# Kernel optimization log

Hardware: AMD Instinct MI355X
Metric: run time of the kernel (lower is better)

Reference implementation:

```python
import jax, jax.numpy as jnp
import numpy as np
from jax import lax

B, S, T = 32, 400, 100
V, OOV = 32000, 100
E, U, AU, GP, ENC = 512, 256, 256, 256, 512


def setup_inputs() -> dict:
    key = jax.random.key(0)
    ks = jax.random.split(key, 24)
    r = lambda k, shp: 0.02 * jax.random.normal(k, shp, dtype=jnp.float32)
    inp = {
        "gt_tokens": jax.random.randint(ks[0], (B, T), 0, V, dtype=jnp.int32),
        "extended_input_tokens": jax.random.randint(ks[1], (B, S), 0, V + OOV, dtype=jnp.int32),
        "enc_output": jax.random.normal(ks[2], (B, S, ENC), dtype=jnp.float32),
        "enc_attn": jax.random.normal(ks[3], (B, S, AU), dtype=jnp.float32),
        "h0": jnp.zeros((B, U), jnp.float32),
        "c0": jnp.zeros((B, U), jnp.float32),
        # learned parameters
        "emb": r(ks[4], (V, E)),
        "lstm_kernel": r(ks[5], (E, 4 * U)),
        "lstm_rec": r(ks[6], (U, 4 * U)),
        "lstm_bias": jnp.zeros((4 * U,), jnp.float32),
        "attn_Wd": r(ks[7], (2 * U, AU)),
        "attn_bd": jnp.zeros((AU,), jnp.float32),
        "attn_Wc": r(ks[8], (1, AU)),
        "attn_Wa": r(ks[9], (AU, 1)),
        "clf_W1": r(ks[10], (U, U)),
        "clf_b1": jnp.zeros((U,), jnp.float32),
        "clf_W2": r(ks[11], (U, V)),
        "clf_b2": jnp.zeros((V,), jnp.float32),
        "gp_Ws": r(ks[12], (2 * U, GP)),
        "gp_Wc": r(ks[13], (ENC, GP)),
        "gp_Wi": r(ks[14], (E, GP)),
        "gp_bi": jnp.zeros((GP,), jnp.float32),
        "gp_Wg": r(ks[15], (GP, 1)),
    }
    return inp


def _decode(gt_tokens, extended_input_tokens, enc_output, enc_attn, h0, c0,
            emb, lstm_kernel, lstm_rec, lstm_bias, attn_Wd, attn_bd, attn_Wc,
            attn_Wa, clf_W1, clf_b1, clf_W2, clf_b2, gp_Ws, gp_Wc, gp_Wi,
            gp_bi, gp_Wg):
    Bn, Sn = extended_input_tokens.shape
    gt_vec = emb[gt_tokens]                      # [B,T,E] teacher-forced inputs
    xs = jnp.swapaxes(gt_vec, 0, 1)              # [T,B,E]
    batch_idx = jnp.arange(Bn)[:, None]

    def step(carry, x):
        h, c, cov = carry                        # [B,U],[B,U],[B,S]
        # single-step LSTM (TF gate order i,f,g,o)
        z = x @ lstm_kernel + h @ lstm_rec + lstm_bias
        i_, f_, g_, o_ = jnp.split(z, 4, axis=-1)
        c = jax.nn.sigmoid(f_) * c + jax.nn.sigmoid(i_) * jnp.tanh(g_)
        h = jax.nn.sigmoid(o_) * jnp.tanh(c)
        dec_state = jnp.concatenate([h, c], axis=1)          # [B,2U]
        # Bahdanau attention with coverage
        dec_attn = dec_state @ attn_Wd + attn_bd             # [B,AU]
        cov_attn = cov[:, :, None] * attn_Wc[0]              # [B,S,AU]
        scores = jnp.tanh(enc_attn + cov_attn + dec_attn[:, None, :]) @ attn_Wa
        a = jax.nn.softmax(scores, axis=1)[:, :, 0]          # [B,S]
        c_vec = jnp.einsum('bse,bs->be', enc_output, a)      # [B,ENC]
        cov_loss = jnp.sum(jnp.minimum(cov, a), axis=1)      # [B]
        cov = cov + a
        # pg: faithful scalar quirk ([0,0,0] of broadcast sum in original)
        g = dec_state[0] @ gp_Ws + c_vec[0] @ gp_Wc + (x[0] @ gp_Wi + gp_bi)
        pg = jax.nn.sigmoid((g @ gp_Wg)[0])
        # vocab distribution, extended with OOV zeros
        vocab_p = jax.nn.softmax((h @ clf_W1 + clf_b1) @ clf_W2 + clf_b2, axis=-1)
        vocab_p = jnp.concatenate([vocab_p, jnp.zeros((Bn, OOV), vocab_p.dtype)], axis=1)
        # copy distribution via scatter-add of attention onto extended ids
        sent_p = jnp.zeros((Bn, V + OOV), a.dtype).at[batch_idx, extended_input_tokens].add(a)
        final = pg * vocab_p + (1.0 - pg) * sent_p           # [B,V+OOV]
        tok = jnp.argmax(final, axis=1).astype(jnp.int32)
        return (h, c, cov), (final, tok, cov_loss)

    cov0 = jnp.zeros((Bn, Sn), jnp.float32)
    _, (probs, seqs, cov_losses) = lax.scan(step, (h0, c0, cov0), xs)
    return (jnp.swapaxes(probs, 0, 1),       # [B,T,V+OOV]
            jnp.swapaxes(seqs, 0, 1),        # [B,T]
            jnp.swapaxes(cov_losses, 0, 1))  # [B,T]


def reference(gt_tokens, extended_input_tokens, enc_output, enc_attn, h0, c0,
              emb, lstm_kernel, lstm_rec, lstm_bias, attn_Wd, attn_bd,
              attn_Wc, attn_Wa, clf_W1, clf_b1, clf_W2, clf_b2, gp_Ws, gp_Wc,
              gp_Wi, gp_bi, gp_Wg):
    return _decode(gt_tokens, extended_input_tokens, enc_output, enc_attn, h0,
                   c0, emb, lstm_kernel, lstm_rec, lstm_bias, attn_Wd,
                   attn_bd, attn_Wc, attn_Wa, clf_W1, clf_b1, clf_W2, clf_b2,
                   gp_Ws, gp_Wc, gp_Wi, gp_bi, gp_Wg)
```

## Files before the change

### kernel.cpp

```cpp
#include <hip/hip_runtime.h>
#include <hip/hip_bf16.h>

#define Bn 32
#define Sn 400
#define Tn 100
#define Vn 32000
#define OOVn 100
#define VEn 32100
#define En 512
#define Un 256
#define AUn 256
#define GPn 256
#define ENCn 512
#define Z4n 1024
#define NPB 250

typedef __attribute__((ext_vector_type(8))) short bf16x8;
typedef __attribute__((ext_vector_type(4))) float f32x4;
typedef unsigned short ushort_t;
typedef unsigned long long u64;

__device__ __forceinline__ float rcp_f(float x){ return __builtin_amdgcn_rcpf(x); }
__device__ __forceinline__ float tanh_fast(float x){
  float e2 = __expf(2.f*x);
  return 1.f - 2.f*rcp_f(e2 + 1.f);
}
__device__ __forceinline__ float sigmoid_f(float x){ return 1.f/(1.f+__expf(-x)); }
__device__ __forceinline__ ushort_t f2bf(float f){
  unsigned u = __float_as_uint(f);
  unsigned r = (u + 0x7FFFu + ((u>>16)&1u)) >> 16;
  return (ushort_t)r;
}
__device__ __forceinline__ u64 shfl_xor_u64(u64 v, int m){
  unsigned lo = (unsigned)v, hi = (unsigned)(v>>32);
  lo = (unsigned)__shfl_xor((int)lo, m);
  hi = (unsigned)__shfl_xor((int)hi, m);
  return ((u64)hi<<32)|(u64)lo;
}

__device__ __forceinline__ void st_rlx(float* p, float v){
  __hip_atomic_store(p, v, __ATOMIC_RELAXED, __HIP_MEMORY_SCOPE_AGENT);
}
__device__ __forceinline__ float ld_rlx(const float* p){
  return __hip_atomic_load(p, __ATOMIC_RELAXED, __HIP_MEMORY_SCOPE_AGENT);
}
__device__ __forceinline__ void st_rlxu(unsigned* p, unsigned v){
  __hip_atomic_store(p, v, __ATOMIC_RELAXED, __HIP_MEMORY_SCOPE_AGENT);
}
__device__ __forceinline__ void st_rlx64(u64* p, u64 v){
  __hip_atomic_store(p, v, __ATOMIC_RELAXED, __HIP_MEMORY_SCOPE_AGENT);
}
__device__ __forceinline__ u64 ld_rlx64(const u64* p){
  return __hip_atomic_load(p, __ATOMIC_RELAXED, __HIP_MEMORY_SCOPE_AGENT);
}
__device__ __forceinline__ void st_flag(unsigned* p, unsigned v){
  __hip_atomic_store(p, v, __ATOMIC_RELAXED, __HIP_MEMORY_SCOPE_AGENT);
}
__device__ __forceinline__ unsigned ld_flag(const unsigned* p){
  return __hip_atomic_load(p, __ATOMIC_RELAXED, __HIP_MEMORY_SCOPE_AGENT);
}


__global__ __launch_bounds__(256) void k_zx(const int* __restrict__ gt,
    const float* __restrict__ emb, const float* __restrict__ Wk,
    const float* __restrict__ bias, float* __restrict__ Zx,
    const float* __restrict__ W2, ushort_t* __restrict__ W2T,
    unsigned* __restrict__ bars, unsigned* __restrict__ bars2,
    float* __restrict__ covloss){
  __shared__ __align__(16) char zbuf[16640];
  float (*As)[17] = (float(*)[17])zbuf;
  float (*Bs)[65] = (float(*)[65])(zbuf + 4352);
  int*   tok_lds  = (int*)(zbuf + 4352 + 4160);
  int r0 = blockIdx.x * 64;
  int c0 = blockIdx.y * 64;
  int tid = threadIdx.x;
  int ty = tid >> 4, tx16 = tid & 15;
  if (blockIdx.x == 0){
    int y = blockIdx.y;
    #pragma unroll
    for (int i = 0; i < 2; ++i){
      int idx = y*512 + i*256 + tid;
      bars[idx] = 0u;
      if (idx < NPB*32) bars2[idx] = 0u;
    }
    if (tid < 200) covloss[y*200 + tid] = 0.f;
  }
  if (tid < 64){
    int r = r0 + tid;
    tok_lds[tid] = gt[(r & 31)*Tn + (r >> 5)];
  }
  __syncthreads();
  float acc[4][4] = {};
  for (int k0 = 0; k0 < En; k0 += 16){
    #pragma unroll
    for (int p = 0; p < 4; ++p){
      int row = (tid>>4) + p*16, kk = tid & 15;
      As[row][kk] = emb[(size_t)tok_lds[row]*En + k0 + kk];
    }
    #pragma unroll
    for (int p = 0; p < 4; ++p){
      int kk = (tid>>6) + p*4, cc = tid & 63;
      Bs[kk][cc] = Wk[(size_t)(k0+kk)*Z4n + c0 + cc];
    }
    __syncthreads();
    #pragma unroll
    for (int kk = 0; kk < 16; ++kk){
      float av[4], bv[4];
      #pragma unroll
      for (int i=0;i<4;++i) av[i] = As[ty*4+i][kk];
      #pragma unroll
      for (int j=0;j<4;++j) bv[j] = Bs[kk][tx16*4+j];
      #pragma unroll
      for (int i=0;i<4;++i)
        #pragma unroll
        for (int j=0;j<4;++j) acc[i][j] += av[i]*bv[j];
    }
    __syncthreads();
  }
  #pragma unroll
  for (int i=0;i<4;++i){
    int row = r0 + ty*4 + i;
    #pragma unroll
    for (int j=0;j<4;++j){
      int col = c0 + tx16*4 + j;
      Zx[(size_t)row*Z4n + col] = acc[i][j] + bias[col];
    }
  }
  float (*tl)[65] = (float(*)[65])zbuf;
  int tx = tid & 63, ty4 = tid >> 6;
  int bid = blockIdx.x*16 + blockIdx.y;
  for (int rep = 0; rep < 3; ++rep){
    int tile = bid + rep*800;
    if (tile >= 2000) break;
    int n0 = (tile % 500) * 64, k0 = (tile / 500) * 64;
    __syncthreads();
    #pragma unroll
    for (int i = 0; i < 16; ++i){
      int kk = ty4 + i*4;
      tl[kk][tx] = W2[(size_t)(k0+kk)*Vn + n0 + tx];
    }
    __syncthreads();
    #pragma unroll
    for (int i = 0; i < 16; ++i){
      int n = ty4 + i*4;
      W2T[(size_t)(n0+n)*Un + k0 + tx] = f2bf(tl[tx][n]);
    }
  }
}


__global__ __launch_bounds__(1024, 1) void k_loop(
    const float* __restrict__ Zx, const float* __restrict__ Wr,
    const float* __restrict__ Wd, const float* __restrict__ bd,
    const float* __restrict__ Wc, const float* __restrict__ Wa,
    const float* __restrict__ enc_attn,
    const float* __restrict__ h0, const float* __restrict__ c0,
    float* __restrict__ h_all, float* __restrict__ decp,
    float* __restrict__ c0_all, float* __restrict__ a_all,
    float* __restrict__ covloss, float* __restrict__ spart,
    unsigned* __restrict__ bars){
  __shared__ float Wr_lds[256*128];
  __shared__ float hfull[Un];
  __shared__ float ppart[8][132];
  __shared__ float zx_lds[128];
  __shared__ float zfull[128];
  __shared__ float hnew[32], cown[32];
  __shared__ float dec_lds[AUn];
  __shared__ float cov_lds[50], sc_lds[50];
  __shared__ float wred[16];
  __shared__ float red8[8];

  const int b = blockIdx.x & 31, k = blockIdx.x >> 5;
  const int tid = threadIdx.x, lane = tid & 63, w = tid >> 6;
  unsigned* flags = bars + b*8*32;
  unsigned* myflag = flags + k*32;

  for (int idx = tid; idx < 256*128; idx += 1024){
    int u = idx >> 7, jl = idx & 127;
    int gcol = 32*k + (jl & 31) + 256*(jl >> 5);
    Wr_lds[idx] = Wr[(size_t)u*Z4n + gcol];
  }
  if (tid < 32) cown[tid] = c0[b*Un + 32*k + tid];
  if (tid < 50) cov_lds[tid] = 0.f;
  const float4 wc4 = *(const float4*)(Wc + lane*4);
  const float4 wa4 = *(const float4*)(Wa + lane*4);
  if (tid < 256) hfull[tid] = h0[b*Un + tid];
  if (tid >= 256 && tid < 384){
    int jl = tid - 256;
    int gcol = 32*k + (jl & 31) + 256*(jl >> 5);
    zx_lds[jl] = Zx[(size_t)(0*Bn + b)*Z4n + gcol];
  }
  __syncthreads();

  {
    int p = tid >> 7, jl = tid & 127;
    float acc = 0.f;
    const float* wr = Wr_lds + (p*32)*128 + jl;
    const float* hb = hfull + p*32;
    #pragma unroll 8
    for (int uu = 0; uu < 32; ++uu) acc += hb[uu]*wr[uu*128];
    ppart[p][jl] = acc;
  }
  __syncthreads();
  if (tid < 128){
    float s = zx_lds[tid];
    #pragma unroll
    for (int q = 0; q < 8; ++q) s += ppart[q][tid];
    zfull[tid] = s;
  }
  __syncthreads();
  if (tid < 32){
    float zi = zfull[tid], zf = zfull[32+tid], zg = zfull[64+tid], zo = zfull[96+tid];
    float cn = sigmoid_f(zf)*cown[tid] + sigmoid_f(zi)*tanhf(zg);
    float hn = sigmoid_f(zo)*tanhf(cn);
    cown[tid] = cn; hnew[tid] = hn;
    int col = 32*k + tid;
    st_rlx(h_all + (size_t)(0*Bn + b)*Un + col, hn);
    if (b == 0) c0_all[0*Un + col] = cn;
  }
  __syncthreads();
  if (tid < 256){
    int c = tid;
    float acc = 0.f;
    const float* wdh = Wd + (size_t)(32*k)*AUn + c;
    #pragma unroll 8
    for (int u = 0; u < 32; ++u) acc += hnew[u]*wdh[(size_t)u*AUn];
    const float* wdc = Wd + (size_t)(Un + 32*k)*AUn + c;
    #pragma unroll 8
    for (int u = 0; u < 32; ++u) acc += cown[u]*wdc[(size_t)u*AUn];
    st_rlx(decp + (size_t)(b*8 + k)*256 + c, acc);
  }
  __syncthreads();
  if (tid == 0) st_flag(myflag, 1u);

  for (int t = 0; t < Tn; ++t){
    const int cur = t & 1, oth = cur ^ 1;
    if (tid < 8){
      while (ld_flag(flags + tid*32) < (unsigned)(t+1))
        __builtin_amdgcn_s_sleep(1);
    }
    __syncthreads();
    if (tid < 256){
      hfull[tid] = ld_rlx(h_all + (size_t)(t*Bn + b)*Un + tid);
    } else if (tid < 512){
      int c = tid - 256;
      float s = bd[c];
      const float* dp = decp + (size_t)cur*(Bn*8*256) + (size_t)(b*8)*256 + c;
      #pragma unroll
      for (int q = 0; q < 8; ++q) s += ld_rlx(dp + q*256);
      dec_lds[c] = s;
    } else if (tid < 520){
      red8[tid-512] = (t > 0) ? ld_rlx(spart + oth*(Bn*8) + b*8 + (tid-512)) : 0.f;
    } else if (tid >= 576 && tid < 704 && t + 1 < Tn){
      int jl = tid - 576;
      int gcol = 32*k + (jl & 31) + 256*(jl >> 5);
      zx_lds[jl] = Zx[(size_t)((t+1)*Bn + b)*Z4n + gcol];
    }
    __syncthreads();
    if (t > 0 && w == 0){
      float pv = (lane < 8) ? red8[lane] : 0.f;
      pv += __shfl_xor(pv, 1); pv += __shfl_xor(pv, 2); pv += __shfl_xor(pv, 4);
      float inv = 1.f / __shfl(pv, 0);
      float clp = 0.f;
      if (lane < 50){
        float aa = sc_lds[lane] * inv;
        float co = cov_lds[lane];
        a_all[(size_t)((t-1)*Bn + b)*Sn + 50*k + lane] = aa;
        clp = fminf(co, aa);
        cov_lds[lane] = co + aa;
      }
      #pragma unroll
      for (int m = 1; m < 64; m <<= 1) clp += __shfl_xor(clp, m);
      if (lane == 0) atomicAdd(&covloss[b*Tn + (t-1)], clp);
    }
    {
      int p = tid >> 7, jl = tid & 127;
      float acc = 0.f;
      const float* wr = Wr_lds + (p*32)*128 + jl;
      const float* hb = hfull + p*32;
      #pragma unroll 8
      for (int uu = 0; uu < 32; ++uu) acc += hb[uu]*wr[uu*128];
      ppart[p][jl] = acc;
    }
    __syncthreads();
    if (tid < 128 && t + 1 < Tn){
      float s = zx_lds[tid];
      #pragma unroll
      for (int q = 0; q < 8; ++q) s += ppart[q][tid];
      zfull[tid] = s;
    }
    __syncthreads();
    if (tid < 32 && t + 1 < Tn){
      float zi = zfull[tid], zf = zfull[32+tid], zg = zfull[64+tid], zo = zfull[96+tid];
      float cn = sigmoid_f(zf)*cown[tid] + sigmoid_f(zi)*tanhf(zg);
      float hn = sigmoid_f(zo)*tanhf(cn);
      cown[tid] = cn; hnew[tid] = hn;
      int col = 32*k + tid;
      st_rlx(h_all + (size_t)((t+1)*Bn + b)*Un + col, hn);
      if (b == 0) c0_all[(t+1)*Un + col] = cn;
    }
    __syncthreads();
    if (w < 4){
      if (t + 1 < Tn){
        int c = tid;
        float acc = 0.f;
        const float* wdh = Wd + (size_t)(32*k)*AUn + c;
        #pragma unroll 8
        for (int u = 0; u < 32; ++u) acc += hnew[u]*wdh[(size_t)u*AUn];
        const float* wdc = Wd + (size_t)(Un + 32*k)*AUn + c;
        #pragma unroll 8
        for (int u = 0; u < 32; ++u) acc += cown[u]*wdc[(size_t)u*AUn];
        st_rlx(decp + (size_t)oth*(Bn*8*256) + (size_t)(b*8 + k)*256 + c, acc);
      }
    } else {
      const float4 da = *(const float4*)(dec_lds + lane*4);
      float wsum = 0.f;
      for (int sl = w - 4; sl < 50; sl += 12){
        float cvv = cov_lds[sl];
        const float4 e = *(const float4*)(enc_attn + ((size_t)(b*Sn + 50*k + sl))*AUn + lane*4);
        float psc = tanh_fast(e.x + cvv*wc4.x + da.x)*wa4.x
                  + tanh_fast(e.y + cvv*wc4.y + da.y)*wa4.y
                  + tanh_fast(e.z + cvv*wc4.z + da.z)*wa4.z
                  + tanh_fast(e.w + cvv*wc4.w + da.w)*wa4.w;
        #pragma unroll
        for (int m = 1; m < 64; m <<= 1) psc += __shfl_xor(psc, m);
        if (lane == 0){
          float ev = __expf(psc);
          sc_lds[sl] = ev;
          wsum += ev;
        }
      }
      if (lane == 0) wred[w] = wsum;
    }
    __syncthreads();
    if (tid == 0){
      float S = 0.f;
      #pragma unroll
      for (int q = 4; q < 16; ++q) S += wred[q];
      st_rlx(spart + cur*(Bn*8) + b*8 + k, S);
    }
    __syncthreads();
    if (tid == 0) st_flag(myflag, (unsigned)(t + 2));
  }

  if (tid < 8){
    while (ld_flag(flags + tid*32) < (unsigned)(Tn + 1))
      __builtin_amdgcn_s_sleep(1);
  }
  __syncthreads();
  if (tid < 8) red8[tid] = ld_rlx(spart + ((Tn-1)&1)*(Bn*8) + b*8 + tid);
  __syncthreads();
  if (w == 0){
    float pv = (lane < 8) ? red8[lane] : 0.f;
    pv += __shfl_xor(pv, 1); pv += __shfl_xor(pv, 2); pv += __shfl_xor(pv, 4);
    float inv = 1.f / __shfl(pv, 0);
    float clp = 0.f;
    if (lane < 50){
      float aa = sc_lds[lane] * inv;
      float co = cov_lds[lane];
      a_all[(size_t)((Tn-1)*Bn + b)*Sn + 50*k + lane] = aa;
      clp = fminf(co, aa);
    }
    #pragma unroll
    for (int m = 1; m < 64; m <<= 1) clp += __shfl_xor(clp, m);
    if (lane == 0) atomicAdd(&covloss[b*Tn + (Tn-1)], clp);
  }
}


__global__ __launch_bounds__(512, 1) void k_post(
    const float* __restrict__ h_all, const float* __restrict__ W1,
    const float* __restrict__ b1, ushort_t* __restrict__ hid,
    const int* __restrict__ gt, const float* __restrict__ emb,
    const float* __restrict__ gpWi, const float* __restrict__ gpbi,
    const float* __restrict__ a_all, const float* __restrict__ enc_out,
    const float* __restrict__ c0_all, const float* __restrict__ gpWs,
    const float* __restrict__ gpWc, const float* __restrict__ gpWg,
    float* __restrict__ pg, const ushort_t* __restrict__ W2T,
    const float* __restrict__ b2, float* __restrict__ Sp,
    float* __restrict__ Ssum, u64* __restrict__ Ap,
    float* __restrict__ probs, unsigned* __restrict__ bars2){
  __shared__ __align__(16) char sb[135168];
  __shared__ float red4[4];
  const int gid = blockIdx.x, tid = threadIdx.x;
  const int lane = tid & 63, w = tid >> 6;
  unsigned* myflag = bars2 + gid*32;

  if (gid < 100){
    int t = gid;
    float* hl = (float*)sb;
    for (int i = tid; i < Bn*Un; i += 512) hl[i] = h_all[(size_t)t*Bn*Un + i];
    __syncthreads();
    int j = tid & 255, p = tid >> 8;
    float bj = b1[j];
    float acc[16];
    #pragma unroll
    for (int i = 0; i < 16; ++i) acc[i] = bj;
    for (int u = 0; u < Un; ++u){
      float wv = W1[u*Un + j];
      const float* hp = hl + (p*16)*Un + u;
      #pragma unroll
      for (int i = 0; i < 16; ++i) acc[i] += hp[i*Un] * wv;
    }
    __syncthreads();
    ushort_t* hidL = (ushort_t*)sb;
    #pragma unroll
    for (int i = 0; i < 16; ++i) hidL[(p*16+i)*Un + j] = f2bf(acc[i]);
    __syncthreads();
    unsigned* hw = (unsigned*)hid + (size_t)t*4096;
    const unsigned* hs = (const unsigned*)hidL;
    for (int i = tid; i < 4096; i += 512) st_rlxu(hw + i, hs[i]);
  } else if (gid < 200){
    int t = gid - 100;
    float* al = (float*)sb;
    float* cv = al + 400;
    float* xl = cv + 512;
    for (int s = tid; s < Sn; s += 512) al[s] = a_all[(size_t)(t*Bn)*Sn + s];
    for (int i = tid; i < En; i += 512) xl[i] = emb[(size_t)gt[t]*En + i];
    __syncthreads();
    if (tid < ENCn){
      float acc = 0.f;
      for (int s = 0; s < Sn; ++s) acc += enc_out[(size_t)s*ENCn + tid]*al[s];
      cv[tid] = acc;
    }
    __syncthreads();
    if (tid < 256){
      int j = tid;
      float g = gpbi[j];
      for (int u = 0; u < En; ++u) g += xl[u]*gpWi[u*GPn + j];
      const float* h0r = h_all + (size_t)t*Bn*Un;
      const float* c0r = c0_all + t*Un;
      for (int u = 0; u < Un; ++u) g += h0r[u]*gpWs[u*GPn + j];
      for (int u = 0; u < Un; ++u) g += c0r[u]*gpWs[(Un+u)*GPn + j];
      for (int e = 0; e < ENCn; ++e) g += cv[e]*gpWc[e*GPn + j];
      float v = g * gpWg[j];
      #pragma unroll
      for (int m = 1; m < 64; m <<= 1) v += __shfl_xor(v, m);
      if (lane == 0) red4[w] = v;
    }
    __syncthreads();
    if (tid == 0)
      st_rlx(&pg[t], 1.f/(1.f+__expf(-(red4[0]+red4[1]+red4[2]+red4[3]))));
  }
  __syncthreads();
  if (tid == 0) st_flag(myflag, 1u);
  if (tid < NPB){ while (ld_flag(bars2 + tid*32) < 1u) __builtin_amdgcn_s_sleep(1); }
  __syncthreads();

  ushort_t* Bs = (ushort_t*)sb;
  const int slice = gid % 125, gx = gid / 125;
  const int n0 = slice * 256;
  {
    int rr = tid >> 1, half = (tid & 1) * 128;
    const ushort_t* gb = W2T + (size_t)(n0 + rr)*Un + half;
    ushort_t* lb = Bs + rr*264 + half;
    #pragma unroll
    for (int j2 = 0; j2 < 16; ++j2)
      *((uint4*)lb + j2) = *((const uint4*)gb + j2);
  }
  __syncthreads();
  const int cbase = gx ? 13 : 0;
  const int nch   = gx ? 12 : 13;

  for (int ci = 0; ci < nch; ++ci){
    int r0 = (cbase + ci) * 128;
    bf16x8 af[8];
    {
      const ushort_t* ar = hid + (size_t)(r0 + w*16 + (lane&15))*Un + (lane>>4)*8;
      #pragma unroll
      for (int kk = 0; kk < 8; ++kk) af[kk] = *(const bf16x8*)(ar + kk*32);
    }
    f32x4 acc[16];
    #pragma unroll
    for (int i = 0; i < 16; ++i) acc[i] = (f32x4){0.f,0.f,0.f,0.f};
    #pragma unroll
    for (int kk = 0; kk < 8; ++kk){
      #pragma unroll
      for (int nt = 0; nt < 16; ++nt){
        bf16x8 bf = *(const bf16x8*)(Bs + (nt*16 + (lane&15))*264 + kk*32 + (lane>>4)*8);
        acc[nt] = __builtin_amdgcn_mfma_f32_16x16x32_bf16(af[kk], bf, acc[nt], 0, 0, 0);
      }
    }
    float rs[4] = {0.f,0.f,0.f,0.f};
    #pragma unroll
    for (int nt = 0; nt < 16; ++nt){
      int v = n0 + nt*16 + (lane&15);
      float b2v = b2[v];
      #pragma unroll
      for (int i = 0; i < 4; ++i) rs[i] += __expf(acc[nt][i] + b2v);
    }
    #pragma unroll
    for (int m = 1; m < 16; m <<= 1)
      #pragma unroll
      for (int i = 0; i < 4; ++i) rs[i] += __shfl_xor(rs[i], m);
    if ((lane&15) == 0){
      int rowloc = w*16 + (lane>>4)*4;
      #pragma unroll
      for (int i = 0; i < 4; ++i)
        st_rlx(&Sp[(size_t)slice*3200 + r0 + rowloc + i], rs[i]);
    }
  }
  __syncthreads();
  if (tid == 0) st_flag(myflag, 2u);
  if (tid < NPB){ while (ld_flag(bars2 + tid*32) < 2u) __builtin_amdgcn_s_sleep(1); }
  __syncthreads();

  if (gid < 7){
    int r = gid*512 + tid;
    if (r < 3200){
      float s = 0.f;
      for (int sl = 0; sl < 125; ++sl) s += ld_rlx(&Sp[(size_t)sl*3200 + r]);
      st_rlx(&Ssum[r], s);
    }
  }
  __syncthreads();
  if (tid == 0) st_flag(myflag, 3u);
  if (tid < NPB){ while (ld_flag(bars2 + tid*32) < 3u) __builtin_amdgcn_s_sleep(1); }
  __syncthreads();

  for (int ci = 0; ci < nch; ++ci){
    int r0 = (cbase + ci) * 128;
    bf16x8 af[8];
    {
      const ushort_t* ar = hid + (size_t)(r0 + w*16 + (lane&15))*Un + (lane>>4)*8;
      #pragma unroll
      for (int kk = 0; kk < 8; ++kk) af[kk] = *(const bf16x8*)(ar + kk*32);
    }
    f32x4 acc[16];
    #pragma unroll
    for (int i = 0; i < 16; ++i) acc[i] = (f32x4){0.f,0.f,0.f,0.f};
    #pragma unroll
    for (int kk = 0; kk < 8; ++kk){
      #pragma unroll
      for (int nt = 0; nt < 16; ++nt){
        bf16x8 bf = *(const bf16x8*)(Bs + (nt*16 + (lane&15))*264 + kk*32 + (lane>>4)*8);
        acc[nt] = __builtin_amdgcn_mfma_f32_16x16x32_bf16(af[kk], bf, acc[nt], 0, 0, 0);
      }
    }
    int rowloc = w*16 + (lane>>4)*4;
    float sc[4]; size_t obase[4];
    #pragma unroll
    for (int i = 0; i < 4; ++i){
      int r = r0 + rowloc + i; int tt = r>>5, bb = r&31;
      sc[i] = ld_rlx(&pg[tt]) / Ssum[r];
      obase[i] = (size_t)(bb*Tn + tt)*VEn;
    }
    u64 pm[4] = {0,0,0,0};
    #pragma unroll
    for (int nt = 0; nt < 16; ++nt){
      int v = n0 + nt*16 + (lane&15);
      float b2v = b2[v];
      #pragma unroll
      for (int i = 0; i < 4; ++i){
        float val = __expf(acc[nt][i] + b2v) * sc[i];
        probs[obase[i] + v] = val;
        u64 p = ((u64)__float_as_uint(val)<<32) | (u64)(0xFFFFFFFFu - (unsigned)v);
        pm[i] = p > pm[i] ? p : pm[i];
      }
    }
    #pragma unroll
    for (int m = 1; m < 16; m <<= 1)
      #pragma unroll
      for (int i = 0; i < 4; ++i){
        u64 o = shfl_xor_u64(pm[i], m);
        pm[i] = o > pm[i] ? o : pm[i];
      }
    if ((lane&15) == 0)
      #pragma unroll
      for (int i = 0; i < 4; ++i)
        st_rlx64(&Ap[(size_t)slice*3200 + r0 + rowloc + i], pm[i]);
  }
}

__global__ __launch_bounds__(256) void k_scatter(const int* __restrict__ ext,
    const float* __restrict__ a_all, const float* __restrict__ pg,
    float* __restrict__ probs, const u64* __restrict__ Ap,
    float* __restrict__ seqs){
  __shared__ int   hkey[1024];
  __shared__ float hval[1024];
  __shared__ u64   wmax[4];
  int r = blockIdx.x; int t = r>>5, b = r&31;
  float c1 = 1.f - pg[t];
  int tid = threadIdx.x;
  #pragma unroll
  for (int i = 0; i < 4; ++i){
    hkey[tid + i*256] = -1;
    hval[tid + i*256] = 0.f;
  }
  size_t obase = (size_t)(b*Tn + t)*VEn;
  if (tid < OOVn) probs[obase + Vn + tid] = 0.f;
  u64 vm = (tid < 125) ? Ap[(size_t)tid*3200 + r] : 0ull;
  __syncthreads();
  for (int s = tid; s < Sn; s += 256){
    int key = ext[b*Sn + s];
    float v = c1 * a_all[(size_t)r*Sn + s];
    unsigned h = ((unsigned)key * 2654435761u) >> 22;
    for (;;){
      int old = atomicCAS(&hkey[h], -1, key);
      if (old == -1 || old == key) break;
      h = (h + 1) & 1023;
    }
    atomicAdd(&hval[h], v);
  }
  __syncthreads();
  u64 pm = vm;
  #pragma unroll
  for (int i = 0; i < 4; ++i){
    int slot = tid + i*256;
    int tk = hkey[slot];
    if (tk >= 0){
      float nv = probs[obase + tk] + hval[slot];
      probs[obase + tk] = nv;
      u64 p = ((u64)__float_as_uint(nv)<<32) | (u64)(0xFFFFFFFFu - (unsigned)tk);
      pm = p > pm ? p : pm;
    }
  }
  #pragma unroll
  for (int m = 1; m < 64; m <<= 1){
    u64 o = shfl_xor_u64(pm, m);
    pm = o > pm ? o : pm;
  }
  int lane = tid & 63, w = tid >> 6;
  if (lane == 0) wmax[w] = pm;
  __syncthreads();
  if (tid == 0){
    u64 mm = wmax[0];
    #pragma unroll
    for (int q = 1; q < 4; ++q) mm = wmax[q] > mm ? wmax[q] : mm;
    unsigned tk = 0xFFFFFFFFu - (unsigned)(mm & 0xFFFFFFFFull);
    seqs[b*Tn + t] = (float)tk;
  }
}


extern "C" void kernel_launch(void* const* d_in, const int* in_sizes, int n_in,
                              void* d_out, int out_size, void* d_ws, size_t ws_size,
                              hipStream_t stream){
  (void)in_sizes; (void)n_in; (void)out_size; (void)ws_size;
  const int*   gt       = (const int*)d_in[0];
  const int*   ext      = (const int*)d_in[1];
  const float* enc_out  = (const float*)d_in[2];
  const float* enc_attn = (const float*)d_in[3];
  const float* h0       = (const float*)d_in[4];
  const float* c0       = (const float*)d_in[5];
  const float* emb      = (const float*)d_in[6];
  const float* Wk       = (const float*)d_in[7];
  const float* Wr       = (const float*)d_in[8];
  const float* lb       = (const float*)d_in[9];
  const float* Wd       = (const float*)d_in[10];
  const float* bd       = (const float*)d_in[11];
  const float* Wc       = (const float*)d_in[12];
  const float* Wa       = (const float*)d_in[13];
  const float* W1       = (const float*)d_in[14];
  const float* b1       = (const float*)d_in[15];
  const float* W2       = (const float*)d_in[16];
  const float* b2       = (const float*)d_in[17];
  const float* gpWs     = (const float*)d_in[18];
  const float* gpWc     = (const float*)d_in[19];
  const float* gpWi     = (const float*)d_in[20];
  const float* gpbi     = (const float*)d_in[21];
  const float* gpWg     = (const float*)d_in[22];

  float* probs   = (float*)d_out;
  float* seqs    = probs + (size_t)Bn*Tn*VEn;
  float* covloss = seqs + Bn*Tn;

  char* wp = (char*)d_ws;
  auto carve = [&](size_t bytes)->void*{
    void* p = (void*)wp; wp += (bytes + 255) & ~(size_t)255; return p;
  };
  float*    Zx      = (float*)carve((size_t)3200*Z4n*4);
  float*    h_all   = (float*)carve((size_t)Tn*Bn*Un*4);
  float*    decp    = (float*)carve((size_t)2*Bn*8*256*4);
  float*    c0_all  = (float*)carve((size_t)Tn*Un*4);
  float*    a_all   = (float*)carve((size_t)3200*Sn*4);
  ushort_t* hid_bf  = (ushort_t*)carve((size_t)3200*Un*2);
  ushort_t* W2T     = (ushort_t*)carve((size_t)Vn*Un*2);
  float*    Ssum    = (float*)carve((size_t)3200*4);
  float*    Sp      = (float*)carve((size_t)125*3200*4);
  u64*      Ap      = (u64*)carve((size_t)125*3200*8);
  float*    pg      = (float*)carve((size_t)Tn*4);
  float*    spart   = (float*)carve((size_t)2*Bn*8*4);
  unsigned* bars    = (unsigned*)carve((size_t)Bn*8*32*4);
  unsigned* bars2   = (unsigned*)carve((size_t)NPB*32*4);

  k_zx  <<<dim3(50,16), 256, 0, stream>>>(gt, emb, Wk, lb, Zx, W2, W2T,
                                          bars, bars2, covloss);

  k_loop<<<256, 1024, 0, stream>>>(Zx, Wr, Wd, bd, Wc, Wa, enc_attn,
                                   h0, c0, h_all, decp, c0_all,
                                   a_all, covloss, spart, bars);

  k_post<<<NPB, 512, 0, stream>>>(h_all, W1, b1, hid_bf, gt, emb,
                                  gpWi, gpbi, a_all, enc_out, c0_all,
                                  gpWs, gpWc, gpWg, pg, W2T, b2,
                                  Sp, Ssum, Ap, probs, bars2);

  k_scatter<<<3200, 256, 0, stream>>>(ext, a_all, pg, probs, Ap, seqs);
}
```

Before: 1.007 ms.

## Move W2 transpose and bf16 conversion into idle k_post blocks

```diff
diff --git a/kernel.cpp b/kernel.cpp
--- a/kernel.cpp
+++ b/kernel.cpp
@@ -64,13 +64,11 @@
 __global__ __launch_bounds__(256) void k_zx(const int* __restrict__ gt,
     const float* __restrict__ emb, const float* __restrict__ Wk,
     const float* __restrict__ bias, float* __restrict__ Zx,
-    const float* __restrict__ W2, ushort_t* __restrict__ W2T,
     unsigned* __restrict__ bars, unsigned* __restrict__ bars2,
     float* __restrict__ covloss){
-  __shared__ __align__(16) char zbuf[16640];
-  float (*As)[17] = (float(*)[17])zbuf;
-  float (*Bs)[65] = (float(*)[65])(zbuf + 4352);
-  int*   tok_lds  = (int*)(zbuf + 4352 + 4160);
+  __shared__ float As[64][17];
+  __shared__ float Bs[16][65];
+  __shared__ int tok_lds[64];
   int r0 = blockIdx.x * 64;
   int c0 = blockIdx.y * 64;
   int tid = threadIdx.x;
@@ -124,26 +122,6 @@
     for (int j=0;j<4;++j){
       int col = c0 + tx16*4 + j;
       Zx[(size_t)row*Z4n + col] = acc[i][j] + bias[col];
-    }
-  }
-  float (*tl)[65] = (float(*)[65])zbuf;
-  int tx = tid & 63, ty4 = tid >> 6;
-  int bid = blockIdx.x*16 + blockIdx.y;
-  for (int rep = 0; rep < 3; ++rep){
-    int tile = bid + rep*800;
-    if (tile >= 2000) break;
-    int n0 = (tile % 500) * 64, k0 = (tile / 500) * 64;
-    __syncthreads();
-    #pragma unroll
-    for (int i = 0; i < 16; ++i){
-      int kk = ty4 + i*4;
-      tl[kk][tx] = W2[(size_t)(k0+kk)*Vn + n0 + tx];
-    }
-    __syncthreads();
-    #pragma unroll
-    for (int i = 0; i < 16; ++i){
-      int n = ty4 + i*4;
-      W2T[(size_t)(n0+n)*Un + k0 + tx] = f2bf(tl[tx][n]);
     }
   }
 }
@@ -376,9 +354,9 @@
     const float* __restrict__ a_all, const float* __restrict__ enc_out,
     const float* __restrict__ c0_all, const float* __restrict__ gpWs,
     const float* __restrict__ gpWc, const float* __restrict__ gpWg,
-    float* __restrict__ pg, const ushort_t* __restrict__ W2T,
-    const float* __restrict__ b2, float* __restrict__ Sp,
-    float* __restrict__ Ssum, u64* __restrict__ Ap,
+    float* __restrict__ pg, const float* __restrict__ W2,
+    ushort_t* __restrict__ W2T, const float* __restrict__ b2,
+    float* __restrict__ Sp, float* __restrict__ Ssum, u64* __restrict__ Ap,
     float* __restrict__ probs, unsigned* __restrict__ bars2){
   __shared__ __align__(16) char sb[135168];
   __shared__ float red4[4];
@@ -441,6 +419,32 @@
     __syncthreads();
     if (tid == 0)
       st_rlx(&pg[t], 1.f/(1.f+__expf(-(red4[0]+red4[1]+red4[2]+red4[3]))));
+  } else {
+    float (*tl)[65] = (float(*)[65])sb;
+    int wblk = gid - 200;
+    for (int rep = 0; rep < 40; ++rep){
+      int tile = wblk*40 + rep;
+      int n0 = (tile % 500) * 64, k0 = (tile / 500) * 64;
+      {
+        int kk = tid >> 6, nn = tid & 63;
+        #pragma unroll
+        for (int i = 0; i < 8; ++i)
+          tl[kk + i*8][nn] = W2[(size_t)(k0 + kk + i*8)*Vn + n0 + nn];
+      }
+      __syncthreads();
+      {
+        int j = tid & 31, n16 = tid >> 5;
+        unsigned* w32 = (unsigned*)W2T;
+        #pragma unroll
+        for (int i = 0; i < 4; ++i){
+          int n = n16 + i*16;
+          unsigned lo = f2bf(tl[2*j][n]);
+          unsigned hi = f2bf(tl[2*j+1][n]);
+          st_rlxu(&w32[(size_t)(n0+n)*128 + (k0>>1) + j], lo | (hi<<16));
+        }
+      }
+      __syncthreads();
+    }
   }
   __syncthreads();
   if (tid == 0) st_flag(myflag, 1u);
@@ -684,7 +688,7 @@
   unsigned* bars    = (unsigned*)carve((size_t)Bn*8*32*4);
   unsigned* bars2   = (unsigned*)carve((size_t)NPB*32*4);
 
-  k_zx  <<<dim3(50,16), 256, 0, stream>>>(gt, emb, Wk, lb, Zx, W2, W2T,
+  k_zx  <<<dim3(50,16), 256, 0, stream>>>(gt, emb, Wk, lb, Zx,
                                           bars, bars2, covloss);
 
   k_loop<<<256, 1024, 0, stream>>>(Zx, Wr, Wd, bd, Wc, Wa, enc_attn,
@@ -693,7 +697,7 @@
 
   k_post<<<NPB, 512, 0, stream>>>(h_all, W1, b1, hid_bf, gt, emb,
                                   gpWi, gpbi, a_all, enc_out, c0_all,
-                                  gpWs, gpWc, gpWg, pg, W2T, b2,
+                                  gpWs, gpWc, gpWg, pg, W2, W2T, b2,
                                   Sp, Ssum, Ap, probs, bars2);
 
   k_scatter<<<3200, 256, 0, stream>>>(ext, a_all, pg, probs, Ap, seqs);
```

Measured after the change: 1.012 ms. No clear change (+0.4%).
